# Kernel tuning notes

Measured on AMD Instinct MI355X. Metric: run time of the kernel, lower is better.

## Reference

```python
import jax, jax.numpy as jnp
import numpy as np

T, B, I, H = 256, 128, 1024, 1024


def setup_inputs() -> dict:
    key = jax.random.key(0)
    ks = jax.random.split(key, 5)
    s = 1.0 / np.sqrt(H)  # PyTorch GRU init scale
    return {
        "x": jax.random.normal(ks[0], (T, B, I), dtype=jnp.float32),
        "w_ih": jax.random.uniform(ks[1], (3 * H, I), jnp.float32, -s, s),
        "w_hh": jax.random.uniform(ks[2], (3 * H, H), jnp.float32, -s, s),
        "b_ih": jax.random.uniform(ks[3], (3 * H,), jnp.float32, -s, s),
        "b_hh": jax.random.uniform(ks[4], (3 * H,), jnp.float32, -s, s),
    }


def reference(x, w_ih, w_hh, b_ih, b_hh):
    # Single-layer GRU over full sequence, h0 = zeros (matches init_hidden).
    # PyTorch gate order in the 3H dim: reset (r), update (z), new (n).
    h_dim = w_hh.shape[1]
    batch = x.shape[1]
    # Precompute all input projections in one big GEMM: [T,B,3H]
    xg = jnp.einsum("tbi,gi->tbg", x, w_ih) + b_ih

    def step(h, xg_t):
        hg = h @ w_hh.T + b_hh  # [B,3H]
        xr, xz, xn = jnp.split(xg_t, 3, axis=-1)
        hr, hz, hn = jnp.split(hg, 3, axis=-1)
        r = jax.nn.sigmoid(xr + hr)
        z = jax.nn.sigmoid(xz + hz)
        n = jnp.tanh(xn + r * hn)
        h_new = (1.0 - z) * n + z * h
        return h_new, h_new

    h0 = jnp.zeros((batch, h_dim), dtype=x.dtype)
    _, outs = jax.lax.scan(step, h0, xg)  # outs: [T,B,H]
    return outs
```

## Files before the change

kernel.cpp:

```cpp
#include <hip/hip_runtime.h>
#include <hip/hip_bf16.h>
#include <cstdint>
#include <cstddef>


typedef __attribute__((ext_vector_type(4))) float f32x4;
typedef __attribute__((ext_vector_type(8))) short s16x8;
typedef __attribute__((ext_vector_type(4))) unsigned short u16x4;

static __device__ __forceinline__ unsigned short f2bf(float f) {
  union { float f; unsigned u; } v; v.f = f;
  unsigned u = v.u;
  u += 0x7FFFu + ((u >> 16) & 1u);
  return (unsigned short)(u >> 16);
}
static __device__ __forceinline__ float bf2f(unsigned short h) {
  union { unsigned u; float f; } v; v.u = ((unsigned)h) << 16;
  return v.f;
}

static __device__ __forceinline__ s16x8 ld16_l2(const unsigned short* p) {
  s16x8 r;
  asm volatile("global_load_dwordx4 %0, %1, off sc0" : "=v"(r) : "v"(p) : "memory");
  return r;
}
static __device__ __forceinline__ void st2_l2(unsigned short* p, unsigned short v) {
  unsigned vv = v;
  asm volatile("global_store_short %0, %1, off sc0" :: "v"(p), "v"(vv) : "memory");
}
static __device__ __forceinline__ s16x8 ld16_mall(const unsigned short* p) {
  s16x8 r;
  asm volatile("global_load_dwordx4 %0, %1, off sc0 sc1" : "=v"(r) : "v"(p) : "memory");
  return r;
}
static __device__ __forceinline__ void st2_mall(unsigned short* p, unsigned short v) {
  unsigned vv = v;
  asm volatile("global_store_short %0, %1, off sc0 sc1" :: "v"(p), "v"(vv) : "memory");
}
static __device__ __forceinline__ void st_flag(unsigned int* p, unsigned v) {
  asm volatile("global_store_dword %0, %1, off sc0 sc1" :: "v"(p), "v"(v) : "memory");
}
static __device__ __forceinline__ unsigned ld_flag(const unsigned int* p) {
  unsigned r;
  asm volatile("global_load_dword %0, %1, off sc0 sc1\n\ts_waitcnt vmcnt(0)"
               : "=v"(r) : "v"(p) : "memory");
  return r;
}
static __device__ __forceinline__ void arrive_l2(unsigned int* p, unsigned v) {
  asm volatile("global_atomic_swap %0, %1, off" :: "v"(p), "v"(v) : "memory");
}
static __device__ __forceinline__ void arrive_mall(unsigned int* p, unsigned v) {
  asm volatile("global_atomic_swap %0, %1, off sc1" :: "v"(p), "v"(v) : "memory");
}
static __device__ __forceinline__ unsigned poll_l2(unsigned int* p, unsigned zero) {
  unsigned old;
  asm volatile("global_atomic_add %0, %1, %2, off sc0\n\ts_waitcnt vmcnt(0)"
               : "=v"(old) : "v"(p), "v"(zero) : "memory");
  return old;
}
static __device__ __forceinline__ unsigned poll_mall(unsigned int* p, unsigned zero) {
  unsigned old;
  asm volatile("global_atomic_add %0, %1, %2, off sc0 sc1\n\ts_waitcnt vmcnt(0)"
               : "=v"(old) : "v"(p), "v"(zero) : "memory");
  return old;
}

__global__ __launch_bounds__(256)
void cvt_bf16(const float* __restrict__ src, unsigned short* __restrict__ dst, int n4) {
  int i = blockIdx.x * 256 + threadIdx.x;
  int stride = gridDim.x * 256;
  for (; i < n4; i += stride) {
    f32x4 v = ((const f32x4*)src)[i];
    u16x4 o = { f2bf(v.x), f2bf(v.y), f2bf(v.z), f2bf(v.w) };
    ((u16x4*)dst)[i] = o;
  }
}

__global__ __launch_bounds__(512, 1)
void gru_scan(const unsigned short* __restrict__ xbf,
              const float* __restrict__ Whh,
              const float* __restrict__ Wih,
              const float* __restrict__ bhh,
              const float* __restrict__ bih,
              float* __restrict__ out,
              unsigned short* __restrict__ hbc,
              unsigned int* __restrict__ bar)
{
  __shared__ char hbuf[32768];
  __shared__ char xbuf[32768];
  __shared__ float part[8][4][64][4];
  __shared__ int fastsh;

  const int tid = threadIdx.x;
  const int lane = tid & 63;
  const int wv = tid >> 6;
  const int id = blockIdx.x;
  const int bg = id & 7;
  const int cg = id >> 3;
  const int c0 = cg * 32;
  const int b0 = bg * 16;
  const int r16 = lane & 15, r4 = lane >> 4;
  const int ks = wv >> 1, nt = wv & 1;

  unsigned int* sflags = bar + (size_t)(bg * 32) * 32;
  unsigned int* dflags = bar + 8192 + bg * 32;

  unsigned myxcc = (__builtin_amdgcn_s_getreg(63508) & 0xFu) | 0x100u;
  if (tid == 0) st_flag(dflags + cg, myxcc);
  if (wv == 0) {
    unsigned v;
    for (;;) {
      v = ld_flag(dflags + (lane & 31));
      if (__ballot(v < 0x100u) == 0) break;
      __builtin_amdgcn_s_sleep(1);
    }
    int bad = (v != myxcc);
    if (tid == 0) fastsh = (__ballot(bad) == 0) ? 1 : 0;
  }
  __syncthreads();
  const bool fast = (fastsh != 0);

  s16x8 bwh[3][8], bwi[3][8];
  #pragma unroll
  for (int n = 0; n < 3; ++n) {
    const float* hrow = Whh + (size_t)(n * 1024 + c0 + nt * 16 + r16) * 1024;
    const float* irow = Wih + (size_t)(n * 1024 + c0 + nt * 16 + r16) * 1024;
    #pragma unroll
    for (int kc = 0; kc < 8; ++kc) {
      int k = ks * 256 + kc * 32 + r4 * 8;
      f32x4 h0 = *(const f32x4*)(hrow + k);
      f32x4 h1 = *(const f32x4*)(hrow + k + 4);
      f32x4 i0 = *(const f32x4*)(irow + k);
      f32x4 i1 = *(const f32x4*)(irow + k + 4);
      s16x8 fh, fi;
      fh[0] = (short)f2bf(h0.x); fh[1] = (short)f2bf(h0.y);
      fh[2] = (short)f2bf(h0.z); fh[3] = (short)f2bf(h0.w);
      fh[4] = (short)f2bf(h1.x); fh[5] = (short)f2bf(h1.y);
      fh[6] = (short)f2bf(h1.z); fh[7] = (short)f2bf(h1.w);
      fi[0] = (short)f2bf(i0.x); fi[1] = (short)f2bf(i0.y);
      fi[2] = (short)f2bf(i0.z); fi[3] = (short)f2bf(i0.w);
      fi[4] = (short)f2bf(i1.x); fi[5] = (short)f2bf(i1.y);
      fi[6] = (short)f2bf(i1.z); fi[7] = (short)f2bf(i1.w);
      bwh[n][kc] = fh;
      bwi[n][kc] = fi;
    }
  }

  const int grow = tid >> 5;
  const int gcolL = tid & 31;
  const int gcol = c0 + gcolL;
  const int g_nt = gcolL >> 4, g_c16 = gcolL & 15;
  const int g_lane = (grow >> 2) * 16 + g_c16;
  const int g_rg = grow & 3;
  const float bR  = bhh[gcol] + bih[gcol];
  const float bZ  = bhh[1024 + gcol] + bih[1024 + gcol];
  const float bNh = bhh[2048 + gcol];
  const float bNx = bih[2048 + gcol];
  float hprev = 0.f;

  const int arow = lane & 15;
  const int aswz = (arow & 7) << 4;
  const int abase = arow * 2048;
  const int g16 = (lane >> 4) * 16;

  const int scb = nt * 1024 + lane * 16;
  int s_goff[4], s_loff[4];
  #pragma unroll
  for (int i = 0; i < 4; ++i) {
    int row = i * 4 + ks;
    s_goff[i] = (b0 + row) * 1024 + (scb >> 1);
    s_loff[i] = row * 2048 + (scb ^ ((row & 7) << 4));
  }

  #pragma unroll
  for (int i = 0; i < 4; ++i)
    *(f32x4*)(hbuf + tid * 64 + i * 16) = (f32x4){0.f, 0.f, 0.f, 0.f};
  {
    s16x8 v0 = *(const s16x8*)(xbf + s_goff[0]);
    s16x8 v1 = *(const s16x8*)(xbf + s_goff[1]);
    s16x8 v2 = *(const s16x8*)(xbf + s_goff[2]);
    s16x8 v3 = *(const s16x8*)(xbf + s_goff[3]);
    *(s16x8*)(xbuf + s_loff[0]) = v0;
    *(s16x8*)(xbuf + s_loff[1]) = v1;
    *(s16x8*)(xbuf + s_loff[2]) = v2;
    *(s16x8*)(xbuf + s_loff[3]) = v3;
  }
  __syncthreads();

  for (int t = 0; t < 256; ++t) {
    f32x4 aR = {0.f,0.f,0.f,0.f}, aZ = aR, aNh = aR, aNx = aR;
    #pragma unroll
    for (int kc = 0; kc < 8; ++kc) {
      int off = (ks * 512 + kc * 64 + g16) ^ aswz;
      s16x8 ah = *(const s16x8*)(hbuf + abase + off);
      s16x8 ax = *(const s16x8*)(xbuf + abase + off);
      aR  = __builtin_amdgcn_mfma_f32_16x16x32_bf16(ah, bwh[0][kc], aR, 0, 0, 0);
      aR  = __builtin_amdgcn_mfma_f32_16x16x32_bf16(ax, bwi[0][kc], aR, 0, 0, 0);
      aZ  = __builtin_amdgcn_mfma_f32_16x16x32_bf16(ah, bwh[1][kc], aZ, 0, 0, 0);
      aZ  = __builtin_amdgcn_mfma_f32_16x16x32_bf16(ax, bwi[1][kc], aZ, 0, 0, 0);
      aNh = __builtin_amdgcn_mfma_f32_16x16x32_bf16(ah, bwh[2][kc], aNh, 0, 0, 0);
      aNx = __builtin_amdgcn_mfma_f32_16x16x32_bf16(ax, bwi[2][kc], aNx, 0, 0, 0);
    }
    *(f32x4*)&part[wv][0][lane][0] = aR;
    *(f32x4*)&part[wv][1][lane][0] = aZ;
    *(f32x4*)&part[wv][2][lane][0] = aNh;
    *(f32x4*)&part[wv][3][lane][0] = aNx;
    __syncthreads();

    {
      float sr = bR, sz = bZ, snh = bNh, snx = bNx;
      #pragma unroll
      for (int kx = 0; kx < 4; ++kx) {
        sr  += part[kx * 2 + g_nt][0][g_lane][g_rg];
        sz  += part[kx * 2 + g_nt][1][g_lane][g_rg];
        snh += part[kx * 2 + g_nt][2][g_lane][g_rg];
        snx += part[kx * 2 + g_nt][3][g_lane][g_rg];
      }
      float rg = 1.f / (1.f + expf(-sr));
      float zg = 1.f / (1.f + expf(-sz));
      float ng = tanhf(snx + rg * snh);
      float h = (1.f - zg) * ng + zg * hprev;
      hprev = h;
      unsigned short* wH = hbc + (size_t)((t + 1) & 1) * 131072;
      size_t widx = (size_t)(b0 + grow) * 1024 + gcol;
      if (fast) st2_l2(wH + widx, f2bf(h));
      else      st2_mall(wH + widx, f2bf(h));
      out[(size_t)t * 131072 + widx] = h;
      asm volatile("s_waitcnt vmcnt(1)" ::: "memory");
    }
    __syncthreads();

    if (tid == 0) {
      if (fast) arrive_l2(sflags + cg * 32, (unsigned)(t + 1));
      else      arrive_mall(sflags + cg * 32, (unsigned)(t + 1));
    }

    if (t < 255) {
      size_t xb = (size_t)(t + 1) * 131072;
      s16x8 x0 = *(const s16x8*)(xbf + xb + s_goff[0]);
      s16x8 x1 = *(const s16x8*)(xbf + xb + s_goff[1]);
      s16x8 x2 = *(const s16x8*)(xbf + xb + s_goff[2]);
      s16x8 x3 = *(const s16x8*)(xbf + xb + s_goff[3]);

      if (wv == 7 && lane < 32) {
        unsigned tgt = (unsigned)(t + 1);
        unsigned int* fp = sflags + lane * 32;
        if (fast) {
          for (;;) {
            unsigned v = poll_l2(fp, 0u);
            if (__ballot(v < tgt) == 0) break;
          }
        } else {
          for (;;) {
            unsigned v = poll_mall(fp, 0u);
            if (__ballot(v < tgt) == 0) break;
            __builtin_amdgcn_s_sleep(1);
          }
        }
      }
      *(s16x8*)(xbuf + s_loff[0]) = x0;
      *(s16x8*)(xbuf + s_loff[1]) = x1;
      *(s16x8*)(xbuf + s_loff[2]) = x2;
      *(s16x8*)(xbuf + s_loff[3]) = x3;
      __syncthreads();

      const unsigned short* hs = hbc + (size_t)((t + 1) & 1) * 131072;
      s16x8 v0, v1, v2, v3;
      if (fast) {
        v0 = ld16_l2(hs + s_goff[0]); v1 = ld16_l2(hs + s_goff[1]);
        v2 = ld16_l2(hs + s_goff[2]); v3 = ld16_l2(hs + s_goff[3]);
      } else {
        v0 = ld16_mall(hs + s_goff[0]); v1 = ld16_mall(hs + s_goff[1]);
        v2 = ld16_mall(hs + s_goff[2]); v3 = ld16_mall(hs + s_goff[3]);
      }
      asm volatile("s_waitcnt vmcnt(0)" ::: "memory");
      *(s16x8*)(hbuf + s_loff[0]) = v0;
      *(s16x8*)(hbuf + s_loff[1]) = v1;
      *(s16x8*)(hbuf + s_loff[2]) = v2;
      *(s16x8*)(hbuf + s_loff[3]) = v3;
      __syncthreads();
    }
  }
}

extern "C" void kernel_launch(void* const* d_in, const int* in_sizes, int n_in,
                              void* d_out, int out_size, void* d_ws, size_t ws_size,
                              hipStream_t stream) {
  const float* x   = (const float*)d_in[0];
  const float* wih = (const float*)d_in[1];
  const float* whh = (const float*)d_in[2];
  const float* bih = (const float*)d_in[3];
  const float* bhh = (const float*)d_in[4];
  float* out = (float*)d_out;

  char* ws = (char*)d_ws;
  unsigned short* xbf = (unsigned short*)ws;
  unsigned short* hbc = (unsigned short*)(ws + 67108864);
  unsigned int*   bar = (unsigned int*)(ws + 67633152);

  hipMemsetAsync(bar, 0, 40960, stream);
  cvt_bf16<<<2048, 256, 0, stream>>>(x, xbf, 32768 * 1024 / 4);
  gru_scan<<<256, 512, 0, stream>>>(xbf, whh, wih, bhh, bih, out, hbc, bar);
}
```

Baseline: 970.5 us.

## Precompute next step's input-projection MFMAs before the barrier wait

```diff
diff --git a/kernel.cpp b/kernel.cpp
--- a/kernel.cpp
+++ b/kernel.cpp
@@ -87,7 +87,6 @@
               unsigned int* __restrict__ bar)
 {
   __shared__ char hbuf[32768];
-  __shared__ char xbuf[32768];
   __shared__ float part[8][4][64][4];
   __shared__ int fastsh;
 
@@ -172,39 +171,39 @@
     s_loff[i] = row * 2048 + (scb ^ ((row & 7) << 4));
   }
 
+  const size_t xrow0 = (size_t)(b0 + r16) * 1024 + ks * 256 + r4 * 8;
+
   #pragma unroll
   for (int i = 0; i < 4; ++i)
     *(f32x4*)(hbuf + tid * 64 + i * 16) = (f32x4){0.f, 0.f, 0.f, 0.f};
+  f32x4 xR = {0.f,0.f,0.f,0.f}, xZ = xR, xNx = xR;
   {
-    s16x8 v0 = *(const s16x8*)(xbf + s_goff[0]);
-    s16x8 v1 = *(const s16x8*)(xbf + s_goff[1]);
-    s16x8 v2 = *(const s16x8*)(xbf + s_goff[2]);
-    s16x8 v3 = *(const s16x8*)(xbf + s_goff[3]);
-    *(s16x8*)(xbuf + s_loff[0]) = v0;
-    *(s16x8*)(xbuf + s_loff[1]) = v1;
-    *(s16x8*)(xbuf + s_loff[2]) = v2;
-    *(s16x8*)(xbuf + s_loff[3]) = v3;
-  }
-  __syncthreads();
-
-  for (int t = 0; t < 256; ++t) {
-    f32x4 aR = {0.f,0.f,0.f,0.f}, aZ = aR, aNh = aR, aNx = aR;
+    s16x8 ax[8];
+    #pragma unroll
+    for (int kc = 0; kc < 8; ++kc)
+      ax[kc] = *(const s16x8*)(xbf + xrow0 + kc * 32);
     #pragma unroll
     for (int kc = 0; kc < 8; ++kc) {
-      int off = (ks * 512 + kc * 64 + g16) ^ aswz;
-      s16x8 ah = *(const s16x8*)(hbuf + abase + off);
-      s16x8 ax = *(const s16x8*)(xbuf + abase + off);
+      xR  = __builtin_amdgcn_mfma_f32_16x16x32_bf16(ax[kc], bwi[0][kc], xR, 0, 0, 0);
+      xZ  = __builtin_amdgcn_mfma_f32_16x16x32_bf16(ax[kc], bwi[1][kc], xZ, 0, 0, 0);
+      xNx = __builtin_amdgcn_mfma_f32_16x16x32_bf16(ax[kc], bwi[2][kc], xNx, 0, 0, 0);
+    }
+  }
+  __syncthreads();
+
+  for (int t = 0; t < 256; ++t) {
+    f32x4 aR = xR, aZ = xZ, aNh = {0.f,0.f,0.f,0.f};
+    #pragma unroll
+    for (int kc = 0; kc < 8; ++kc) {
+      s16x8 ah = *(const s16x8*)(hbuf + abase + ((ks * 512 + kc * 64 + g16) ^ aswz));
       aR  = __builtin_amdgcn_mfma_f32_16x16x32_bf16(ah, bwh[0][kc], aR, 0, 0, 0);
-      aR  = __builtin_amdgcn_mfma_f32_16x16x32_bf16(ax, bwi[0][kc], aR, 0, 0, 0);
       aZ  = __builtin_amdgcn_mfma_f32_16x16x32_bf16(ah, bwh[1][kc], aZ, 0, 0, 0);
-      aZ  = __builtin_amdgcn_mfma_f32_16x16x32_bf16(ax, bwi[1][kc], aZ, 0, 0, 0);
       aNh = __builtin_amdgcn_mfma_f32_16x16x32_bf16(ah, bwh[2][kc], aNh, 0, 0, 0);
-      aNx = __builtin_amdgcn_mfma_f32_16x16x32_bf16(ax, bwi[2][kc], aNx, 0, 0, 0);
     }
     *(f32x4*)&part[wv][0][lane][0] = aR;
     *(f32x4*)&part[wv][1][lane][0] = aZ;
     *(f32x4*)&part[wv][2][lane][0] = aNh;
-    *(f32x4*)&part[wv][3][lane][0] = aNx;
+    *(f32x4*)&part[wv][3][lane][0] = xNx;
     __syncthreads();
 
     {
@@ -236,11 +235,19 @@
     }
 
     if (t < 255) {
-      size_t xb = (size_t)(t + 1) * 131072;
-      s16x8 x0 = *(const s16x8*)(xbf + xb + s_goff[0]);
-      s16x8 x1 = *(const s16x8*)(xbf + xb + s_goff[1]);
-      s16x8 x2 = *(const s16x8*)(xbf + xb + s_goff[2]);
-      s16x8 x3 = *(const s16x8*)(xbf + xb + s_goff[3]);
+      const unsigned short* xsrc = xbf + (size_t)(t + 1) * 131072 + xrow0;
+      s16x8 ax[8];
+      #pragma unroll
+      for (int kc = 0; kc < 8; ++kc)
+        ax[kc] = *(const s16x8*)(xsrc + kc * 32);
+      f32x4 nR = {0.f,0.f,0.f,0.f}, nZ = nR, nNx = nR;
+      #pragma unroll
+      for (int kc = 0; kc < 8; ++kc) {
+        nR  = __builtin_amdgcn_mfma_f32_16x16x32_bf16(ax[kc], bwi[0][kc], nR, 0, 0, 0);
+        nZ  = __builtin_amdgcn_mfma_f32_16x16x32_bf16(ax[kc], bwi[1][kc], nZ, 0, 0, 0);
+        nNx = __builtin_amdgcn_mfma_f32_16x16x32_bf16(ax[kc], bwi[2][kc], nNx, 0, 0, 0);
+      }
+      xR = nR; xZ = nZ; xNx = nNx;
 
       if (wv == 7 && lane < 32) {
         unsigned tgt = (unsigned)(t + 1);
@@ -258,10 +265,6 @@
           }
         }
       }
-      *(s16x8*)(xbuf + s_loff[0]) = x0;
-      *(s16x8*)(xbuf + s_loff[1]) = x1;
-      *(s16x8*)(xbuf + s_loff[2]) = x2;
-      *(s16x8*)(xbuf + s_loff[3]) = x3;
       __syncthreads();
 
       const unsigned short* hs = hbc + (size_t)((t + 1) & 1) * 131072;
```

Measured after the change: 1.240 ms. 27.8% more time.
